# Kernel tuning notes

Hardware: AMD Instinct MI355X
Metric: run time of the kernel (lower is better)

The kernel has to match this reference:

```python
import jax, jax.numpy as jnp
import numpy as np

STRIDE = 4.0      # fpn_strides[0]
POOL = 7          # roi_align_size
SR = 2            # roi_align_sampling_ratio
NUM_CLASSES = 10
B, N = 2, 512
C, H, W = 256, 256, 256
OUT = 1024


def _bilinear(feat_hwc, y, x):
    # feat_hwc: [H, W, C]; y, x: [N, 7, 7, SR, SR] sample coords (feature units)
    Hf, Wf, _ = feat_hwc.shape
    valid = (y > -1.0) & (y < Hf) & (x > -1.0) & (x < Wf)
    y = jnp.clip(y, 0.0, Hf - 1.0)
    x = jnp.clip(x, 0.0, Wf - 1.0)
    y0 = jnp.floor(y)
    x0 = jnp.floor(x)
    y0i = y0.astype(jnp.int32)
    x0i = x0.astype(jnp.int32)
    y1i = jnp.minimum(y0i + 1, Hf - 1)
    x1i = jnp.minimum(x0i + 1, Wf - 1)
    ly = (y - y0)[..., None]
    lx = (x - x0)[..., None]
    hy = 1.0 - ly
    hx = 1.0 - lx
    v = (hy * hx * feat_hwc[y0i, x0i] + hy * lx * feat_hwc[y0i, x1i]
         + ly * hx * feat_hwc[y1i, x0i] + ly * lx * feat_hwc[y1i, x1i])
    return v * valid[..., None]


def _roi_align_rotated(feat_hwc, boxes):
    # boxes: [N, 5] = (cx, cy, w, h, theta) in feature coords -> [N, 7, 7, C]
    cx, cy, w, h, th = (boxes[:, k] for k in range(5))
    bins = jnp.arange(POOL, dtype=feat_hwc.dtype)
    sub = (jnp.arange(SR, dtype=feat_hwc.dtype) + 0.5) / SR
    # local (box-frame) coords of sample points along each axis: [N, 7, SR]
    ys = -h[:, None, None] / 2 + (h / POOL)[:, None, None] * (bins[None, :, None] + sub[None, None, :])
    xs = -w[:, None, None] / 2 + (w / POOL)[:, None, None] * (bins[None, :, None] + sub[None, None, :])
    yy = ys[:, :, None, :, None]  # [N,7,1,SR,1]
    xx = xs[:, None, :, None, :]  # [N,1,7,1,SR]
    cos = jnp.cos(th)[:, None, None, None, None]
    sin = jnp.sin(th)[:, None, None, None, None]
    gx = cx[:, None, None, None, None] + xx * cos - yy * sin
    gy = cy[:, None, None, None, None] + xx * sin + yy * cos
    v = _bilinear(feat_hwc, gy, gx)  # [N,7,7,SR,SR,C]
    return v.mean(axis=(3, 4))       # average-pool the SRxSR samples per bin


def norm_angle(a):
    return (a + jnp.pi / 2) % jnp.pi - jnp.pi / 2


def setup_inputs():
    key = jax.random.key(0)
    ks = jax.random.split(key, 14)
    feat = jax.random.normal(ks[0], (B, C, H, W), jnp.float32)
    cx = jax.random.uniform(ks[1], (B, N), minval=16.0, maxval=H - 16.0)
    cy = jax.random.uniform(ks[2], (B, N), minval=16.0, maxval=W - 16.0)
    bw = jax.random.uniform(ks[3], (B, N), minval=8.0, maxval=64.0)
    bh = jax.random.uniform(ks[4], (B, N), minval=8.0, maxval=64.0)
    th = jax.random.uniform(ks[5], (B, N), minval=-np.pi / 2, maxval=np.pi / 2)
    proposals = jnp.stack([cx, cy, bw, bh, th], axis=-1).astype(jnp.float32)
    d_in = C * POOL * POOL
    s = 0.02
    return {
        'feat': feat,
        'proposals': proposals,
        'W1': jax.random.normal(ks[6], (d_in, OUT), jnp.float32) * s,
        'b1': jnp.zeros((OUT,), jnp.float32),
        'W2': jax.random.normal(ks[7], (OUT, OUT), jnp.float32) * s,
        'b2': jnp.zeros((OUT,), jnp.float32),
        'Wcls': jax.random.normal(ks[8], (OUT, NUM_CLASSES + 1), jnp.float32) * s,
        'bcls': jnp.zeros((NUM_CLASSES + 1,), jnp.float32),
        'Wreg': jax.random.normal(ks[9], (OUT, 5), jnp.float32) * s,
        'breg': jnp.zeros((5,), jnp.float32),
    }


def reference(feat, proposals, W1, b1, W2, b2, Wcls, bcls, Wreg, breg):
    Bn, Nn = proposals.shape[:2]
    feat_hwc = jnp.transpose(feat, (0, 2, 3, 1))  # [B,H,W,C]
    pooled = jax.vmap(_roi_align_rotated)(feat_hwc, proposals)  # [B,N,7,7,C]
    # torch flattens [N, C, 7, 7] -> C*49; match that layout
    x = jnp.transpose(pooled, (0, 1, 4, 2, 3)).reshape(Bn, Nn, -1)
    x = jax.nn.relu(x @ W1 + b1)
    x = jax.nn.relu(x @ W2 + b2)
    cls = x @ Wcls + bcls   # [B,N,11]
    reg = x @ Wreg + breg   # [B,N,5]
    # decode (proposals scaled to image coords by stride; theta unscaled)
    scale = jnp.array([STRIDE, STRIDE, STRIDE, STRIDE, 1.0], feat.dtype)
    p = proposals * scale
    clamp_v = float(abs(np.log(16.0 / 1000.0)))
    bx = p[..., 2] * reg[..., 0] + p[..., 0]
    by = p[..., 3] * reg[..., 1] + p[..., 1]
    bw = p[..., 2] * jnp.exp(jnp.clip(reg[..., 2], -clamp_v, clamp_v))
    bh = p[..., 3] * jnp.exp(jnp.clip(reg[..., 3], -clamp_v, clamp_v))
    ba = norm_angle(p[..., 4] + reg[..., 4])
    boxes = jnp.stack([bx, by, bw, bh, ba], axis=-1)
    return boxes, cls
```

## Files before the change

kernel.cpp:

```cpp
#include <hip/hip_runtime.h>
#include <math.h>
#include <stdint.h>

#define BB 2
#define NN 512
#define CC 256
#define HH 256
#define WW 256
#define DIN 12544
#define OUT1 1024
#define NCLS 11
#define NROI 1024
#define SK1 8
#define SK2 2
#define NWB 1696

typedef short bf16x8 __attribute__((ext_vector_type(8)));
typedef float f32x4 __attribute__((ext_vector_type(4)));

__device__ inline unsigned short f2bf(float f) {
  unsigned int u = __float_as_uint(f);
  u += 0x7FFF + ((u >> 16) & 1);
  return (unsigned short)(u >> 16);
}
__device__ inline float bf2f(unsigned short h) {
  return __uint_as_float(((unsigned int)h) << 16);
}
__device__ inline float4 ld_bf4(const unsigned short* p) {
  ushort4 r = *(const ushort4*)p;
  return make_float4(bf2f(r.x), bf2f(r.y), bf2f(r.z), bf2f(r.w));
}

__device__ inline void gll16(const void* g, void* l) {
  __builtin_amdgcn_global_load_lds(
      reinterpret_cast<const __attribute__((address_space(1))) void*>(
          reinterpret_cast<uintptr_t>(g)),
      reinterpret_cast<__attribute__((address_space(3))) void*>(
          (unsigned int)reinterpret_cast<uintptr_t>(l)),
      16, 0, 0);
}

__global__ __launch_bounds__(256) void prep_feat(
    const float* __restrict__ feat, unsigned short* __restrict__ fhwc) {
  __shared__ unsigned short tile[64 * 132];
  int bid = blockIdx.x;
  int tid = threadIdx.x;
  int hw0 = (bid & 511) * 128;
  int c0 = ((bid >> 9) & 3) * 64;
  int b = bid >> 11;
  int cl_base = tid >> 5;
  int hwq = (tid & 31) * 4;
#pragma unroll
  for (int pass = 0; pass < 8; ++pass) {
    int cl = cl_base + pass * 8;
    float4 v = *(const float4*)(feat + ((size_t)b * CC + c0 + cl) * (HH * WW) +
                                hw0 + hwq);
    ushort4 o;
    o.x = f2bf(v.x); o.y = f2bf(v.y); o.z = f2bf(v.z); o.w = f2bf(v.w);
    *(ushort4*)&tile[cl * 132 + hwq] = o;
  }
  __syncthreads();
  int hi = tid >> 4, lo = tid & 15;
#pragma unroll
  for (int pass = 0; pass < 8; ++pass) {
    int hwl = hi + pass * 16;
    int cq = lo * 4;
    ushort4 o;
    o.x = tile[(cq + 0) * 132 + hwl];
    o.y = tile[(cq + 1) * 132 + hwl];
    o.z = tile[(cq + 2) * 132 + hwl];
    o.w = tile[(cq + 3) * 132 + hwl];
    *(ushort4*)(fhwc + ((size_t)b * (HH * WW) + hw0 + hwl) * CC + c0 + cq) = o;
  }
}

__device__ inline void bilin(float gy, float gx, int& y0, int& x0, int& y1,
                             int& x1, float& w00, float& w01, float& w10,
                             float& w11) {
  float valid = (gy > -1.f && gy < 256.f && gx > -1.f && gx < 256.f) ? 0.25f : 0.f;
  float y = fminf(fmaxf(gy, 0.f), 255.f);
  float x = fminf(fmaxf(gx, 0.f), 255.f);
  float yf = floorf(y), xf = floorf(x);
  y0 = (int)yf; x0 = (int)xf;
  y1 = min(y0 + 1, 255); x1 = min(x0 + 1, 255);
  float ly = y - yf, lx = x - xf, hy = 1.f - ly, hx = 1.f - lx;
  w00 = hy * hx * valid; w01 = hy * lx * valid;
  w10 = ly * hx * valid; w11 = ly * lx * valid;
}

__global__ __launch_bounds__(256) void roi_fused(
    const unsigned short* __restrict__ fhwc, const float* __restrict__ props,
    unsigned short* __restrict__ pooled, const float* __restrict__ W1,
    unsigned short* __restrict__ W1T, const float* __restrict__ W2,
    unsigned short* __restrict__ W2T, int roi_cnt) {
  __shared__ unsigned short tile[64 * 132];
  int bid = blockIdx.x;
  int tid = threadIdx.x;

  if (bid >= roi_cnt) {
    int u = bid - roi_cnt;
    const float* in;
    unsigned short* out;
    int Kout, kblk, nblk;
    bool perm;
    if (u < 1568) {
      in = W1; out = W1T; Kout = DIN; kblk = u % 196; nblk = u / 196;
      perm = true;
    } else {
      u -= 1568;
      in = W2; out = W2T; Kout = OUT1; kblk = u & 15; nblk = u >> 4;
      perm = false;
    }
    int k0 = kblk * 64, n0 = nblk * 128;
    int kl_base = tid >> 5;
    int nq = (tid & 31) * 4;
#pragma unroll
    for (int pass = 0; pass < 8; ++pass) {
      int kl = kl_base + pass * 8;
      int k = k0 + kl;
      int row = perm ? ((k & 255) * 49 + (k >> 8)) : k;
      float4 v = *(const float4*)(in + (size_t)row * OUT1 + n0 + nq);
      ushort4 o;
      o.x = f2bf(v.x); o.y = f2bf(v.y); o.z = f2bf(v.z); o.w = f2bf(v.w);
      *(ushort4*)&tile[kl * 132 + nq] = o;
    }
    __syncthreads();
    int hi = tid >> 4, lo = tid & 15;
#pragma unroll
    for (int pass = 0; pass < 8; ++pass) {
      int nl = hi + pass * 16;
      int kq = lo * 4;
      ushort4 o;
      o.x = tile[(kq + 0) * 132 + nl];
      o.y = tile[(kq + 1) * 132 + nl];
      o.z = tile[(kq + 2) * 132 + nl];
      o.w = tile[(kq + 3) * 132 + nl];
      *(ushort4*)(out + (size_t)(n0 + nl) * Kout + k0 + kq) = o;
    }
    return;
  }

  int roi = bid >> 1;
  int half = bid & 1;
  int b = roi >> 9;
  const float* p = props + (size_t)roi * 5;
  float cx = p[0], cy = p[1], w = p[2], h = p[3], th = p[4];
  float sn = sinf(th), cs = cosf(th);
  int wave = tid >> 6, lane = tid & 63;
  int c4 = lane * 4;
  const unsigned short* fb = fhwc + (size_t)b * HH * WW * CC;
  unsigned short* outp = pooled + (size_t)roi * DIN;

  for (int bin = half * 4 + wave; bin < 49; bin += 8) {
    int py = bin / 7, px = bin - py * 7;
    float a0 = 0.f, a1 = 0.f, a2 = 0.f, a3 = 0.f;
#pragma unroll
    for (int sy = 0; sy < 2; ++sy) {
#pragma unroll
      for (int sx = 0; sx < 2; ++sx) {
        float ys = -0.5f * h + (h / 7.0f) * ((float)py + ((float)sy + 0.5f) * 0.5f);
        float xs = -0.5f * w + (w / 7.0f) * ((float)px + ((float)sx + 0.5f) * 0.5f);
        float gx = cx + xs * cs - ys * sn;
        float gy = cy + xs * sn + ys * cs;
        int y0, x0, y1, x1; float w00, w01, w10, w11;
        bilin(gy, gx, y0, x0, y1, x1, w00, w01, w10, w11);
        float4 v00 = ld_bf4(fb + ((size_t)(y0 * WW + x0)) * CC + c4);
        float4 v01 = ld_bf4(fb + ((size_t)(y0 * WW + x1)) * CC + c4);
        float4 v10 = ld_bf4(fb + ((size_t)(y1 * WW + x0)) * CC + c4);
        float4 v11 = ld_bf4(fb + ((size_t)(y1 * WW + x1)) * CC + c4);
        a0 += w00 * v00.x + w01 * v01.x + w10 * v10.x + w11 * v11.x;
        a1 += w00 * v00.y + w01 * v01.y + w10 * v10.y + w11 * v11.y;
        a2 += w00 * v00.z + w01 * v01.z + w10 * v10.z + w11 * v11.z;
        a3 += w00 * v00.w + w01 * v01.w + w10 * v10.w + w11 * v11.w;
      }
    }
    ushort4 o;
    o.x = f2bf(a0); o.y = f2bf(a1); o.z = f2bf(a2); o.w = f2bf(a3);
    *(ushort4*)(outp + bin * 256 + c4) = o;
  }
}

__global__ __launch_bounds__(256) void roi_align_nchw(
    const float* __restrict__ feat, const float* __restrict__ props,
    unsigned short* __restrict__ pooled) {
  int roi = blockIdx.x;
  int b = roi >> 9;
  int c = threadIdx.x;
  const float* p = props + (size_t)roi * 5;
  float cx = p[0], cy = p[1], w = p[2], h = p[3], th = p[4];
  float sn = sinf(th), cs = cosf(th);
  const float* fb = feat + ((size_t)b * CC + c) * (HH * WW);
  unsigned short* outp = pooled + (size_t)roi * DIN;
  for (int bin = 0; bin < 49; ++bin) {
    int py = bin / 7, px = bin - py * 7;
    float acc = 0.f;
#pragma unroll
    for (int sy = 0; sy < 2; ++sy) {
#pragma unroll
      for (int sx = 0; sx < 2; ++sx) {
        float ys = -0.5f * h + (h / 7.0f) * ((float)py + ((float)sy + 0.5f) * 0.5f);
        float xs = -0.5f * w + (w / 7.0f) * ((float)px + ((float)sx + 0.5f) * 0.5f);
        float gx = cx + xs * cs - ys * sn;
        float gy = cy + xs * sn + ys * cs;
        int y0, x0, y1, x1; float w00, w01, w10, w11;
        bilin(gy, gx, y0, x0, y1, x1, w00, w01, w10, w11);
        acc += w00 * fb[(size_t)y0 * WW + x0] + w01 * fb[(size_t)y0 * WW + x1] +
               w10 * fb[(size_t)y1 * WW + x0] + w11 * fb[(size_t)y1 * WW + x1];
      }
    }
    outp[bin * 256 + c] = f2bf(acc);
  }
}

__global__ __launch_bounds__(256) void gemm_mfma_128(
    const unsigned short* __restrict__ A, const unsigned short* __restrict__ Bw,
    float* __restrict__ part, int K, int Ks) {
  __shared__ short As[128 * 32];
  __shared__ short Bs[128 * 32];
  int tid = threadIdx.x;
  int w = tid >> 6, lane = tid & 63;
  int quad = lane >> 4, l16 = lane & 15;
  int m0 = blockIdx.y * 128, n0 = blockIdx.x * 128;
  int bz = blockIdx.z;
  int wm = w >> 1, wn = w & 1;

  const char* pA = (const char*)A +
      ((size_t)(m0 + 32 * w + (lane >> 2)) * K + (size_t)bz * Ks) * 2 +
      (lane & 3) * 16;
  const char* pB = (const char*)Bw +
      ((size_t)(n0 + 32 * w + (lane >> 2)) * K + (size_t)bz * Ks) * 2 +
      (lane & 3) * 16;
  short* la = &As[w * 1024];
  short* lb = &Bs[w * 1024];
  const size_t rstep = (size_t)K * 2 * 16;

  f32x4 acc[4][4] = {};
  int aoff[4], boff[4];
#pragma unroll
  for (int t = 0; t < 4; ++t) {
    aoff[t] = (wm * 64 + t * 16 + l16) * 32 + quad * 8;
    boff[t] = (wn * 64 + t * 16 + l16) * 32 + quad * 8;
  }

  for (int kk = 0; kk < Ks; kk += 32) {
    __syncthreads();
    gll16(pA, la);
    gll16(pA + rstep, la + 512);
    gll16(pB, lb);
    gll16(pB + rstep, lb + 512);
    pA += 64; pB += 64;
    __syncthreads();
    bf16x8 af[4], bfr[4];
#pragma unroll
    for (int t = 0; t < 4; ++t) af[t] = *(const bf16x8*)&As[aoff[t]];
#pragma unroll
    for (int t = 0; t < 4; ++t) bfr[t] = *(const bf16x8*)&Bs[boff[t]];
#pragma unroll
    for (int mt = 0; mt < 4; ++mt)
#pragma unroll
      for (int nt = 0; nt < 4; ++nt)
        acc[mt][nt] = __builtin_amdgcn_mfma_f32_16x16x32_bf16(
            af[mt], bfr[nt], acc[mt][nt], 0, 0, 0);
  }

  float* pp = part + (size_t)bz * (OUT1 * NROI);
#pragma unroll
  for (int mt = 0; mt < 4; ++mt)
#pragma unroll
    for (int nt = 0; nt < 4; ++nt) {
      int col = n0 + wn * 64 + nt * 16 + l16;
#pragma unroll
      for (int r = 0; r < 4; ++r) {
        int row = m0 + wm * 64 + mt * 16 + quad * 4 + r;
        pp[(size_t)row * OUT1 + col] = acc[mt][nt][r];
      }
    }
}

__global__ __launch_bounds__(256) void reduce_relu_bf16(
    const float* __restrict__ part, const float* __restrict__ bias,
    unsigned short* __restrict__ out) {
  int i = blockIdx.x * 256 + threadIdx.x;
  int base = i * 4;
  int col = base & (OUT1 - 1);
  const float4* p = (const float4*)part;
  float4 s = p[i];
#pragma unroll
  for (int z = 1; z < SK1; ++z) {
    float4 t = p[i + (size_t)z * (NROI * OUT1 / 4)];
    s.x += t.x; s.y += t.y; s.z += t.z; s.w += t.w;
  }
  float4 bv = *(const float4*)(bias + col);
  ushort4 o;
  o.x = f2bf(fmaxf(s.x + bv.x, 0.f));
  o.y = f2bf(fmaxf(s.y + bv.y, 0.f));
  o.z = f2bf(fmaxf(s.z + bv.z, 0.f));
  o.w = f2bf(fmaxf(s.w + bv.w, 0.f));
  *(ushort4*)(out + base) = o;
}

__global__ __launch_bounds__(256) void gemm_mfma_64_part(
    const unsigned short* __restrict__ A, const unsigned short* __restrict__ Bw,
    float* __restrict__ part, int K, int Ks) {
  __shared__ short As[64 * 64];
  __shared__ short Bs[64 * 64];
  int tid = threadIdx.x;
  int w = tid >> 6, lane = tid & 63;
  int quad = lane >> 4, l16 = lane & 15;
  int m0 = blockIdx.y * 64, n0 = blockIdx.x * 64;
  int bz = blockIdx.z;
  int wm = w >> 1, wn = w & 1;

  const char* pA = (const char*)A +
      ((size_t)(m0 + 16 * w + (lane >> 3)) * K + (size_t)bz * Ks) * 2 +
      (lane & 7) * 16;
  const char* pB = (const char*)Bw +
      ((size_t)(n0 + 16 * w + (lane >> 3)) * K + (size_t)bz * Ks) * 2 +
      (lane & 7) * 16;
  short* la = &As[w * 1024];
  short* lb = &Bs[w * 1024];
  const size_t rstep = (size_t)K * 2 * 8;

  f32x4 acc[2][2] = {};
  int aoff[2], boff[2];
#pragma unroll
  for (int t = 0; t < 2; ++t) {
    aoff[t] = (wm * 32 + t * 16 + l16) * 64 + quad * 8;
    boff[t] = (wn * 32 + t * 16 + l16) * 64 + quad * 8;
  }

  for (int kk = 0; kk < Ks; kk += 64) {
    __syncthreads();
    gll16(pA, la);
    gll16(pA + rstep, la + 512);
    gll16(pB, lb);
    gll16(pB + rstep, lb + 512);
    pA += 128; pB += 128;
    __syncthreads();
#pragma unroll
    for (int ks = 0; ks < 2; ++ks) {
      bf16x8 af[2], bfr[2];
#pragma unroll
      for (int t = 0; t < 2; ++t) af[t] = *(const bf16x8*)&As[aoff[t] + ks * 32];
#pragma unroll
      for (int t = 0; t < 2; ++t) bfr[t] = *(const bf16x8*)&Bs[boff[t] + ks * 32];
#pragma unroll
      for (int mt = 0; mt < 2; ++mt)
#pragma unroll
        for (int nt = 0; nt < 2; ++nt)
          acc[mt][nt] = __builtin_amdgcn_mfma_f32_16x16x32_bf16(
              af[mt], bfr[nt], acc[mt][nt], 0, 0, 0);
    }
  }
  float* pp = part + (size_t)bz * (OUT1 * NROI);
#pragma unroll
  for (int mt = 0; mt < 2; ++mt)
#pragma unroll
    for (int nt = 0; nt < 2; ++nt) {
      int col = n0 + wn * 32 + nt * 16 + l16;
#pragma unroll
      for (int r = 0; r < 4; ++r) {
        int row = m0 + wm * 32 + mt * 16 + quad * 4 + r;
        pp[(size_t)row * OUT1 + col] = acc[mt][nt][r];
      }
    }
}

__global__ __launch_bounds__(256) void head_kernel(
    const float* __restrict__ P0, const float* __restrict__ P1,
    const float* __restrict__ b2, const float* __restrict__ Wcls,
    const float* __restrict__ bcls, const float* __restrict__ Wreg,
    const float* __restrict__ breg, const float* __restrict__ props,
    float* __restrict__ out) {
  __shared__ float xrow[1024];
  __shared__ float partial[16][17];
  __shared__ float res[16];
  int row = blockIdx.x;
  int tid = threadIdx.x;
  {
    size_t off = (size_t)row * 1024 + tid * 4;
    float4 a = *(const float4*)(P0 + off);
    float4 b = *(const float4*)(P1 + off);
    float4 bv = *(const float4*)(b2 + tid * 4);
    xrow[tid * 4 + 0] = fmaxf(a.x + b.x + bv.x, 0.f);
    xrow[tid * 4 + 1] = fmaxf(a.y + b.y + bv.y, 0.f);
    xrow[tid * 4 + 2] = fmaxf(a.z + b.z + bv.z, 0.f);
    xrow[tid * 4 + 3] = fmaxf(a.w + b.w + bv.w, 0.f);
  }
  __syncthreads();
  int col = tid & 15, slice = tid >> 4;
  float s = 0.f;
  if (col < NCLS) {
    for (int k = slice * 64; k < slice * 64 + 64; ++k)
      s += xrow[k] * Wcls[(size_t)k * NCLS + col];
  } else {
    int rc = col - NCLS;
    for (int k = slice * 64; k < slice * 64 + 64; ++k)
      s += xrow[k] * Wreg[(size_t)k * 5 + rc];
  }
  partial[slice][col] = s;
  __syncthreads();
  if (tid < 16) {
    float t = 0.f;
    for (int sl = 0; sl < 16; ++sl) t += partial[sl][tid];
    t += (tid < NCLS) ? bcls[tid] : breg[tid - NCLS];
    res[tid] = t;
  }
  __syncthreads();
  if (tid < NCLS) out[5120 + (size_t)row * NCLS + tid] = res[tid];
  if (tid == 0) {
    const float* p = props + (size_t)row * 5;
    float p0 = p[0] * 4.f, p1 = p[1] * 4.f, p2 = p[2] * 4.f, p3 = p[3] * 4.f,
          p4 = p[4];
    float r0 = res[11], r1 = res[12], r2 = res[13], r3 = res[14], r4 = res[15];
    const float V = 4.135166556742356f;
    float bx = p2 * r0 + p0;
    float by = p3 * r1 + p1;
    float bw = p2 * expf(fminf(fmaxf(r2, -V), V));
    float bh = p3 * expf(fminf(fmaxf(r3, -V), V));
    const float PI = 3.14159265358979323846f;
    float a = p4 + r4;
    float m = fmodf(a + PI * 0.5f, PI);
    if (m < 0.f) m += PI;
    float ba = m - PI * 0.5f;
    float* bo = out + (size_t)row * 5;
    bo[0] = bx; bo[1] = by; bo[2] = bw; bo[3] = bh; bo[4] = ba;
  }
}

extern "C" void kernel_launch(void* const* d_in, const int* in_sizes, int n_in,
                              void* d_out, int out_size, void* d_ws,
                              size_t ws_size, hipStream_t stream) {
  const float* feat  = (const float*)d_in[0];
  const float* props = (const float*)d_in[1];
  const float* W1    = (const float*)d_in[2];
  const float* b1    = (const float*)d_in[3];
  const float* W2    = (const float*)d_in[4];
  const float* b2    = (const float*)d_in[5];
  const float* Wcls  = (const float*)d_in[6];
  const float* bcls  = (const float*)d_in[7];
  const float* Wreg  = (const float*)d_in[8];
  const float* breg  = (const float*)d_in[9];
  float* out = (float*)d_out;

  char* wp = (char*)d_ws;
  unsigned short* pooled = (unsigned short*)wp; wp += (size_t)NROI * DIN * 2;
  unsigned short* W1T    = (unsigned short*)wp; wp += (size_t)OUT1 * DIN * 2;
  unsigned short* W2T    = (unsigned short*)wp; wp += (size_t)OUT1 * OUT1 * 2;
  unsigned short* x1     = (unsigned short*)wp; wp += (size_t)NROI * OUT1 * 2;
  float*          part1  = (float*)wp;          wp += (size_t)SK1 * NROI * OUT1 * 4;
  float*          part2  = (float*)wp;          wp += (size_t)SK2 * NROI * OUT1 * 4;
  unsigned short* fhwc   = (unsigned short*)wp;

  size_t need_min  = (size_t)(wp - (char*)d_ws);
  size_t need_full = need_min + (size_t)BB * CC * HH * WW * 2;

  if (ws_size >= need_full) {
    prep_feat<<<BB * 4 * (HH * WW / 128), 256, 0, stream>>>(feat, fhwc);
    roi_fused<<<NROI * 2 + NWB, 256, 0, stream>>>(fhwc, props, pooled, W1, W1T,
                                                  W2, W2T, NROI * 2);
  } else {
    roi_fused<<<NWB, 256, 0, stream>>>(fhwc, props, pooled, W1, W1T, W2, W2T,
                                       0);
    roi_align_nchw<<<NROI, 256, 0, stream>>>(feat, props, pooled);
  }

  gemm_mfma_128<<<dim3(8, 8, SK1), 256, 0, stream>>>(pooled, W1T, part1, DIN,
                                                     DIN / SK1);
  reduce_relu_bf16<<<NROI * OUT1 / 1024, 256, 0, stream>>>(part1, b1, x1);
  gemm_mfma_64_part<<<dim3(16, 16, SK2), 256, 0, stream>>>(x1, W2T, part2, OUT1,
                                                           OUT1 / SK2);
  head_kernel<<<NROI, 256, 0, stream>>>(part2, part2 + (size_t)NROI * OUT1, b2,
                                        Wcls, bcls, Wreg, breg, props, out);
}
```

Baseline: 378.7 us.

## Split W1 transpose into two coalesced passes and restructure feature transpose

The W1 fp32-to-bf16 transpose, which used a strided row permutation, becomes two steps. First a plain coalesced transpose into a natural-order bf16 buffer runs in the prep kernel. Then a per-row permutation pass inside the ROI kernel reorders the 12544 elements through LDS. The feature NCHW-to-NHWC conversion now handles all 256 channels per block with a 64KB LDS tile and 16-byte stores, and is merged with the W1/W2 weight conversion into one launch. This should cut uncoalesced global reads and improve store width. The cost is an extra workspace buffer, an extra read/write of W1, and larger LDS use that lowers occupancy.

```diff
diff --git a/kernel.cpp b/kernel.cpp
--- a/kernel.cpp
+++ b/kernel.cpp
@@ -13,7 +13,6 @@
 #define NROI 1024
 #define SK1 8
 #define SK2 2
-#define NWB 1696
 
 typedef short bf16x8 __attribute__((ext_vector_type(8)));
 typedef float f32x4 __attribute__((ext_vector_type(4)));
@@ -40,37 +39,72 @@
       16, 0, 0);
 }
 
-__global__ __launch_bounds__(256) void prep_feat(
-    const float* __restrict__ feat, unsigned short* __restrict__ fhwc) {
-  __shared__ unsigned short tile[64 * 132];
+__global__ __launch_bounds__(256) void prep_kernel(
+    const float* __restrict__ feat, unsigned short* __restrict__ fhwc,
+    const float* __restrict__ W1, unsigned short* __restrict__ W1nat,
+    const float* __restrict__ W2, unsigned short* __restrict__ W2T,
+    int n_feat) {
+  __shared__ unsigned short smem[128 * 256];
   int bid = blockIdx.x;
   int tid = threadIdx.x;
-  int hw0 = (bid & 511) * 128;
-  int c0 = ((bid >> 9) & 3) * 64;
-  int b = bid >> 11;
-  int cl_base = tid >> 5;
-  int hwq = (tid & 31) * 4;
+
+  if (bid < n_feat) {
+    int hw0 = (bid & 511) * 128;
+    int b = bid >> 9;
+    const float* src = feat + ((size_t)b * CC + tid) * (HH * WW) + hw0;
+#pragma unroll 8
+    for (int i = 0; i < 32; ++i) {
+      float4 v = *(const float4*)(src + i * 4);
+      smem[(i * 4 + 0) * 256 + tid] = f2bf(v.x);
+      smem[(i * 4 + 1) * 256 + tid] = f2bf(v.y);
+      smem[(i * 4 + 2) * 256 + tid] = f2bf(v.z);
+      smem[(i * 4 + 3) * 256 + tid] = f2bf(v.w);
+    }
+    __syncthreads();
+    unsigned short* dst = fhwc + ((size_t)b * (HH * WW) + hw0) * CC;
+#pragma unroll
+    for (int p = 0; p < 16; ++p) {
+      int chunk = p * 256 + tid;
+      uint4 v = *(const uint4*)&smem[chunk * 8];
+      *(uint4*)(dst + chunk * 8) = v;
+    }
+    return;
+  }
+
+  int u = bid - n_feat;
+  const float* in;
+  unsigned short* out;
+  int Kout, kblk, nblk;
+  if (u < 1568) {
+    in = W1; out = W1nat; Kout = DIN; kblk = u % 196; nblk = u / 196;
+  } else {
+    u -= 1568;
+    in = W2; out = W2T; Kout = OUT1; kblk = u & 15; nblk = u >> 4;
+  }
+  unsigned short* tile = smem;
+  int k0 = kblk * 64, n0 = nblk * 128;
+  int kl_base = tid >> 5;
+  int nq = (tid & 31) * 4;
 #pragma unroll
   for (int pass = 0; pass < 8; ++pass) {
-    int cl = cl_base + pass * 8;
-    float4 v = *(const float4*)(feat + ((size_t)b * CC + c0 + cl) * (HH * WW) +
-                                hw0 + hwq);
+    int kl = kl_base + pass * 8;
+    float4 v = *(const float4*)(in + (size_t)(k0 + kl) * OUT1 + n0 + nq);
     ushort4 o;
     o.x = f2bf(v.x); o.y = f2bf(v.y); o.z = f2bf(v.z); o.w = f2bf(v.w);
-    *(ushort4*)&tile[cl * 132 + hwq] = o;
+    *(ushort4*)&tile[kl * 132 + nq] = o;
   }
   __syncthreads();
   int hi = tid >> 4, lo = tid & 15;
 #pragma unroll
   for (int pass = 0; pass < 8; ++pass) {
-    int hwl = hi + pass * 16;
-    int cq = lo * 4;
+    int nl = hi + pass * 16;
+    int kq = lo * 4;
     ushort4 o;
-    o.x = tile[(cq + 0) * 132 + hwl];
-    o.y = tile[(cq + 1) * 132 + hwl];
-    o.z = tile[(cq + 2) * 132 + hwl];
-    o.w = tile[(cq + 3) * 132 + hwl];
-    *(ushort4*)(fhwc + ((size_t)b * (HH * WW) + hw0 + hwl) * CC + c0 + cq) = o;
+    o.x = tile[(kq + 0) * 132 + nl];
+    o.y = tile[(kq + 1) * 132 + nl];
+    o.z = tile[(kq + 2) * 132 + nl];
+    o.w = tile[(kq + 3) * 132 + nl];
+    *(ushort4*)(out + (size_t)(n0 + nl) * Kout + k0 + kq) = o;
   }
 }
 
@@ -90,52 +124,43 @@
 
 __global__ __launch_bounds__(256) void roi_fused(
     const unsigned short* __restrict__ fhwc, const float* __restrict__ props,
-    unsigned short* __restrict__ pooled, const float* __restrict__ W1,
-    unsigned short* __restrict__ W1T, const float* __restrict__ W2,
-    unsigned short* __restrict__ W2T, int roi_cnt) {
-  __shared__ unsigned short tile[64 * 132];
+    unsigned short* __restrict__ pooled,
+    const unsigned short* __restrict__ W1nat,
+    unsigned short* __restrict__ W1T, int roi_cnt) {
+  __shared__ unsigned short rbuf[12544];
   int bid = blockIdx.x;
   int tid = threadIdx.x;
 
   if (bid >= roi_cnt) {
-    int u = bid - roi_cnt;
-    const float* in;
-    unsigned short* out;
-    int Kout, kblk, nblk;
-    bool perm;
-    if (u < 1568) {
-      in = W1; out = W1T; Kout = DIN; kblk = u % 196; nblk = u / 196;
-      perm = true;
-    } else {
-      u -= 1568;
-      in = W2; out = W2T; Kout = OUT1; kblk = u & 15; nblk = u >> 4;
-      perm = false;
-    }
-    int k0 = kblk * 64, n0 = nblk * 128;
-    int kl_base = tid >> 5;
-    int nq = (tid & 31) * 4;
-#pragma unroll
-    for (int pass = 0; pass < 8; ++pass) {
-      int kl = kl_base + pass * 8;
-      int k = k0 + kl;
-      int row = perm ? ((k & 255) * 49 + (k >> 8)) : k;
-      float4 v = *(const float4*)(in + (size_t)row * OUT1 + n0 + nq);
-      ushort4 o;
-      o.x = f2bf(v.x); o.y = f2bf(v.y); o.z = f2bf(v.z); o.w = f2bf(v.w);
-      *(ushort4*)&tile[kl * 132 + nq] = o;
+    int n = bid - roi_cnt;
+    const unsigned short* src = W1nat + (size_t)n * DIN;
+#pragma unroll
+    for (int p = 0; p < 6; ++p) {
+      int idx = p * 256 + tid;
+      *(uint4*)&rbuf[idx * 8] = *(const uint4*)(src + idx * 8);
+    }
+    if (tid < 32) {
+      int idx = 1536 + tid;
+      *(uint4*)&rbuf[idx * 8] = *(const uint4*)(src + idx * 8);
     }
     __syncthreads();
-    int hi = tid >> 4, lo = tid & 15;
-#pragma unroll
-    for (int pass = 0; pass < 8; ++pass) {
-      int nl = hi + pass * 16;
-      int kq = lo * 4;
-      ushort4 o;
-      o.x = tile[(kq + 0) * 132 + nl];
-      o.y = tile[(kq + 1) * 132 + nl];
-      o.z = tile[(kq + 2) * 132 + nl];
-      o.w = tile[(kq + 3) * 132 + nl];
-      *(ushort4*)(out + (size_t)(n0 + nl) * Kout + k0 + kq) = o;
+    unsigned short* dst = W1T + (size_t)n * DIN;
+#pragma unroll
+    for (int p = 0; p < 7; ++p) {
+      int chunk = p * 256 + tid;
+      if (chunk < 1568) {
+        int bin = chunk >> 5;
+        int c0 = (chunk & 31) * 8;
+        unsigned int o[8];
+#pragma unroll
+        for (int e = 0; e < 8; ++e) o[e] = rbuf[(c0 + e) * 49 + bin];
+        uint4 v;
+        v.x = o[0] | (o[1] << 16);
+        v.y = o[2] | (o[3] << 16);
+        v.z = o[4] | (o[5] << 16);
+        v.w = o[6] | (o[7] << 16);
+        *(uint4*)(dst + chunk * 8) = v;
+      }
     }
     return;
   }
@@ -450,18 +475,20 @@
   unsigned short* x1     = (unsigned short*)wp; wp += (size_t)NROI * OUT1 * 2;
   float*          part1  = (float*)wp;          wp += (size_t)SK1 * NROI * OUT1 * 4;
   float*          part2  = (float*)wp;          wp += (size_t)SK2 * NROI * OUT1 * 4;
+  unsigned short* W1nat  = (unsigned short*)wp; wp += (size_t)OUT1 * DIN * 2;
   unsigned short* fhwc   = (unsigned short*)wp;
 
   size_t need_min  = (size_t)(wp - (char*)d_ws);
   size_t need_full = need_min + (size_t)BB * CC * HH * WW * 2;
 
   if (ws_size >= need_full) {
-    prep_feat<<<BB * 4 * (HH * WW / 128), 256, 0, stream>>>(feat, fhwc);
-    roi_fused<<<NROI * 2 + NWB, 256, 0, stream>>>(fhwc, props, pooled, W1, W1T,
-                                                  W2, W2T, NROI * 2);
+    prep_kernel<<<1024 + 1696, 256, 0, stream>>>(feat, fhwc, W1, W1nat, W2,
+                                                 W2T, 1024);
+    roi_fused<<<2048 + 1024, 256, 0, stream>>>(fhwc, props, pooled, W1nat, W1T,
+                                               2048);
   } else {
-    roi_fused<<<NWB, 256, 0, stream>>>(fhwc, props, pooled, W1, W1T, W2, W2T,
-                                       0);
+    prep_kernel<<<1696, 256, 0, stream>>>(feat, fhwc, W1, W1nat, W2, W2T, 0);
+    roi_fused<<<1024, 256, 0, stream>>>(fhwc, props, pooled, W1nat, W1T, 0);
     roi_align_nchw<<<NROI, 256, 0, stream>>>(feat, props, pooled);
   }
 
```

Result: slower. 397.9 us (+5.1%).
